# Optimization experiments

Hardware: AMD Instinct MI355X
Metric: run time of the kernel (lower is better)

The kernel has to match this reference:

```python
import jax, jax.numpy as jnp
import numpy as np

B, S, D, C = 2, 4096, 768, 8192
SCALE = 1.0
LN_EPS = 1e-5


def setup_inputs() -> dict:
    key = jax.random.key(0)
    ks = jax.random.split(key, 8)
    std = 0.03
    return {
        "x": jax.random.normal(ks[0], (B, S, D), dtype=jnp.float32),
        "attention_masks": jax.random.randint(ks[1], (B, S), 0, 2).astype(jnp.int32),
        "Wk": jax.random.normal(ks[2], (D, D), dtype=jnp.float32) * std,
        "Wv": jax.random.normal(ks[3], (D, D), dtype=jnp.float32) * std,
        "bv": jnp.zeros((D,), dtype=jnp.float32),
        "Q": jax.random.normal(ks[4], (C, D), dtype=jnp.float32) * std,  # label_representations
        "ln_gamma": jnp.ones((D,), dtype=jnp.float32),
        "ln_beta": jnp.zeros((D,), dtype=jnp.float32),
        "w_out": jax.random.normal(ks[5], (D,), dtype=jnp.float32) * std,  # output_linear.weight [1, D]
        "b_out": jnp.zeros((), dtype=jnp.float32),  # output_linear.bias [1]
    }


def reference(x, attention_masks, Wk, Wv, bv, Q, ln_gamma, ln_beta, w_out, b_out):
    # K, V projections (torch Linear: x @ W.T + b)
    K = jnp.einsum("bsd,ed->bse", x, Wk)
    V = jnp.einsum("bsd,ed->bse", x, Wv) + bv
    # label-query cross-attention scores: [B, C, S]
    scores = jnp.einsum("cd,bsd->bcs", Q, K)
    # additive mask: -inf where attention_masks == 0 (intended semantics of pad/repeat/masked_fill)
    scores = jnp.where(attention_masks[:, None, :] == 0, -jnp.inf, scores)
    attn = jax.nn.softmax(scores / SCALE, axis=2)  # [B, C, S]
    y = jnp.einsum("bcs,bsd->bcd", attn, V)  # [B, C, D]
    # LayerNorm over last dim
    mu = jnp.mean(y, axis=-1, keepdims=True)
    var = jnp.mean((y - mu) ** 2, axis=-1, keepdims=True)
    y = (y - mu) * jax.lax.rsqrt(var + LN_EPS) * ln_gamma + ln_beta
    # elementwise weight-mul-sum output head: [B, C]
    return jnp.einsum("bcd,d->bc", y, w_out) + b_out
```

## Files before the change

### kernel.cpp

```cpp
#include <hip/hip_runtime.h>
#include <hip/hip_bf16.h>
#include <hip/hip_fp16.h>

typedef _Float16 f16x8 __attribute__((ext_vector_type(8)));
typedef _Float16 f16x4 __attribute__((ext_vector_type(4)));
typedef float f32x4 __attribute__((ext_vector_type(4)));

#define AS1 __attribute__((address_space(1)))
#define AS3 __attribute__((address_space(3)))
#define MFMA16(a, b, c) __builtin_amdgcn_mfma_f32_16x16x32_f16(a, b, c, 0, 0, 0)
#define BARRIER asm volatile("s_barrier" ::: "memory")

__global__ __launch_bounds__(256) void maskscan(const int* __restrict__ am,
                                                int* __restrict__ idx,
                                                int* __restrict__ meta) {
  const int b = blockIdx.x, t = threadIdx.x;
  const int* m = am + (size_t)b * 4096;
  int* ix = idx + (size_t)b * 4096;
  __shared__ int cnt[256];
  __shared__ int pre[257];
  int loc[16], c = 0;
#pragma unroll
  for (int j = 0; j < 16; ++j) {
    loc[j] = m[t * 16 + j];
    c += (loc[j] != 0);
  }
  cnt[t] = c;
  __syncthreads();
  if (t == 0) {
    pre[0] = 0;
    for (int i = 0; i < 256; ++i) pre[i + 1] = pre[i] + cnt[i];
  }
  __syncthreads();
  int p = pre[t];
#pragma unroll
  for (int j = 0; j < 16; ++j)
    if (loc[j]) ix[p++] = t * 16 + j;
  const int valid = pre[256];
  int nsp = ((valid + 255) >> 8) << 8;
  if (nsp < 256) nsp = 256;
  for (int j = valid + t; j < nsp; j += 256) ix[j] = -1;
  if (t == 0) { meta[2 * b] = valid; meta[2 * b + 1] = nsp; }
}

__global__ __launch_bounds__(192) void gather_cvt(const float* __restrict__ x,
                                                  const int* __restrict__ idx,
                                                  const int* __restrict__ meta,
                                                  unsigned short* __restrict__ xc) {
  const int b = blockIdx.y, row = blockIdx.x, t = threadIdx.x;
  if (row >= meta[2 * b + 1]) return;
  const int src = idx[(size_t)b * 4096 + row];
  unsigned short* dst = xc + ((size_t)b * 4096 + row) * 768 + t * 4;
  f16x4 h;
  if (src < 0) {
    h[0] = h[1] = h[2] = h[3] = (_Float16)0.0f;
  } else {
    float4 v = *(const float4*)(x + ((size_t)b * 4096 + src) * 768 + t * 4);
    h[0] = (_Float16)v.x; h[1] = (_Float16)v.y; h[2] = (_Float16)v.z; h[3] = (_Float16)v.w;
  }
  *(f16x4*)dst = h;
}

__global__ __launch_bounds__(256) void cvt_f32_f16(const float* __restrict__ in,
                                                   unsigned short* __restrict__ out,
                                                   int n8) {
  int i = blockIdx.x * 256 + threadIdx.x;
  if (i >= n8) return;
  const float4* p = (const float4*)in + 2 * (size_t)i;
  float4 a = p[0], b = p[1];
  f16x8 h;
  h[0] = (_Float16)a.x; h[1] = (_Float16)a.y; h[2] = (_Float16)a.z; h[3] = (_Float16)a.w;
  h[4] = (_Float16)b.x; h[5] = (_Float16)b.y; h[6] = (_Float16)b.z; h[7] = (_Float16)b.w;
  *(f16x8*)(out + (size_t)i * 8) = h;
}

template <int OMODE, bool RBIAS, int EXITD>
__global__ __launch_bounds__(256) void gemm_nt(const unsigned short* __restrict__ A, int lda,
                                               const unsigned short* __restrict__ B, int ldb,
                                               void* __restrict__ Cout, int ldc,
                                               const float* __restrict__ bias,
                                               const int* __restrict__ meta,
                                               int N, int K) {
  const int nbn = N >> 7;
  const int bm = blockIdx.x / nbn, bn = blockIdx.x % nbn;
  if constexpr (EXITD == 1) {
    if (((bm & 31) << 7) >= meta[2 * (bm >> 5) + 1]) return;
  } else if constexpr (EXITD == 2) {
    if (((bn & 31) << 7) >= meta[2 * (bn >> 5) + 1]) return;
  }
  __shared__ __attribute__((aligned(16))) unsigned short As[128 * 64];
  __shared__ __attribute__((aligned(16))) unsigned short Bs[128 * 64];
  const int tid = threadIdx.x;
  const int w = tid >> 6, l = tid & 63;
  const int wr = w >> 1, wc = w & 1;
  const int lr = l & 15, lg = l >> 4;

  const unsigned short* Ab = A + (size_t)bm * 128 * lda;
  const unsigned short* Bb = B + (size_t)bn * 128 * ldb;

  f32x4 acc[4][4] = {};

  auto ldfrag = [&](const unsigned short* base, int row, int kk) {
    int off = row * 128 + kk * 64 + lg * 16;
    off ^= (row & 7) << 4;
    return *(const f16x8*)((const unsigned char*)base + off);
  };

  for (int kt = 0; kt < K; kt += 64) {
#pragma unroll
    for (int i = 0; i < 4; ++i) {
      const int c = i * 256 + w * 64 + l;
      const int row = c >> 3, col = (((c & 7) ^ (row & 7)) << 3);
      __builtin_amdgcn_global_load_lds((const AS1 void*)(Ab + (size_t)row * lda + kt + col),
                                       (AS3 void*)(As + (i * 256 + w * 64) * 8), 16, 0, 0);
    }
#pragma unroll
    for (int i = 0; i < 4; ++i) {
      const int c = i * 256 + w * 64 + l;
      const int row = c >> 3, col = (((c & 7) ^ (row & 7)) << 3);
      __builtin_amdgcn_global_load_lds((const AS1 void*)(Bb + (size_t)row * ldb + kt + col),
                                       (AS3 void*)(Bs + (i * 256 + w * 64) * 8), 16, 0, 0);
    }
    __syncthreads();
#pragma unroll
    for (int kk = 0; kk < 2; ++kk) {
      f16x8 af[4], bf[4];
#pragma unroll
      for (int mi = 0; mi < 4; ++mi) af[mi] = ldfrag(As, wr * 64 + mi * 16 + lr, kk);
#pragma unroll
      for (int ni = 0; ni < 4; ++ni) bf[ni] = ldfrag(Bs, wc * 64 + ni * 16 + lr, kk);
#pragma unroll
      for (int mi = 0; mi < 4; ++mi)
#pragma unroll
        for (int ni = 0; ni < 4; ++ni)
          acc[mi][ni] = __builtin_amdgcn_mfma_f32_16x16x32_f16(af[mi], bf[ni], acc[mi][ni], 0, 0, 0);
    }
    __syncthreads();
  }

#pragma unroll
  for (int mi = 0; mi < 4; ++mi) {
#pragma unroll
    for (int r = 0; r < 4; ++r) {
      const int row = bm * 128 + wr * 64 + mi * 16 + lg * 4 + r;
      const float badd = RBIAS ? bias[row] : 0.0f;
#pragma unroll
      for (int ni = 0; ni < 4; ++ni) {
        const int col = bn * 128 + wc * 64 + ni * 16 + lr;
        float v = acc[mi][ni][r] + badd;
        if constexpr (OMODE == 0)
          ((unsigned short*)Cout)[(size_t)row * ldc + col] =
              __builtin_bit_cast(unsigned short, (_Float16)v);
        else
          ((float*)Cout)[(size_t)row * ldc + col] = v;
      }
    }
  }
}

template <int EPI, int KSP>
__global__ __launch_bounds__(256, 2) void gemmk(
    const unsigned short* __restrict__ A, int lda,
    const unsigned short* __restrict__ B, int ldb,
    unsigned short* __restrict__ Cout, int ldc, size_t sCk,
    const int* __restrict__ meta, int NTfix,
    int XC, int WBM, int WBN) {
  constexpr int RA = 4;
  constexpr int RB = 2;
  constexpr int BUFSZ = 16384 + 8192;
  __shared__ __attribute__((aligned(16))) unsigned char lds[3 * BUFSZ];

  const int tid = threadIdx.x;
  const int wv = tid >> 6, l = tid & 63;
  const int wm = wv >> 1, wn = wv & 1;
  const int lr = l & 15, lg = l >> 4;

  const int ks = blockIdx.y;
  const int valid = meta[0], nsp = meta[1];

  const int bid = blockIdx.x;
  const int xcd = bid & 7, ii = bid >> 3;
  const int bm = (xcd / XC) * WBM + ii / WBN;
  const int bn = (ii % WBN) * XC + (xcd % XC);

  int NT, koff;
  if constexpr (EPI == 2) {
    NT = NTfix; koff = 0;
    if ((bn << 7) >= nsp) return;
  } else {
    NT = (nsp / KSP) >> 5;
    koff = ks * (nsp / KSP);
  }

  const unsigned short* Ab = A + koff + (size_t)bm * 256 * lda;
  const unsigned short* Bb = B + koff + (size_t)(bn * 128) * ldb;

  const int xr = ((lr >> 1) & 3) << 4;
  const int aoff = ((wm * 128 + lr) << 6) + ((lg << 4) ^ xr);
  const int boff = 16384 + ((wn * 64 + lr) << 6) + ((lg << 4) ^ xr);

  const int scol = ((tid & 3) ^ ((tid >> 3) & 3)) << 3;
  const int srow = tid >> 2;
  const unsigned short* sa[RA];
  const unsigned short* sb[RB];
#pragma unroll
  for (int r = 0; r < RA; ++r) sa[r] = Ab + (size_t)(srow + r * 64) * lda + scol;
#pragma unroll
  for (int r = 0; r < RB; ++r) sb[r] = Bb + (size_t)(srow + r * 64) * ldb + scol;
  const int dA = wv * 1024;

  auto stageAll = [&](int eoff, int bo_) {
#pragma unroll
    for (int r = 0; r < RA; ++r)
      __builtin_amdgcn_global_load_lds((const AS1 void*)(sa[r] + eoff),
                                       (AS3 void*)(lds + bo_ + r * 4096 + dA), 16, 0, 0);
#pragma unroll
    for (int r = 0; r < RB; ++r)
      __builtin_amdgcn_global_load_lds((const AS1 void*)(sb[r] + eoff),
                                       (AS3 void*)(lds + bo_ + 16384 + r * 4096 + dA), 16, 0, 0);
  };

  f32x4 acc[8][4] = {};

  stageAll(0, 0);
  stageAll(32, BUFSZ);
  asm volatile("s_waitcnt vmcnt(6)" ::: "memory");
  BARRIER;

  int bo = 0;
  for (int t = 0; t < NT; ++t) {
    const unsigned char* pa = lds + bo + aoff;
    const unsigned char* pb = lds + bo + boff;
    f16x8 a0 = *(const f16x8*)(pa);
    f16x8 a1 = *(const f16x8*)(pa + 1024);
    f16x8 a2 = *(const f16x8*)(pa + 2048);
    f16x8 a3 = *(const f16x8*)(pa + 3072);
    f16x8 b0 = *(const f16x8*)(pb);
    f16x8 b1 = *(const f16x8*)(pb + 1024);
    f16x8 b2 = *(const f16x8*)(pb + 2048);
    f16x8 b3 = *(const f16x8*)(pb + 3072);
    const int bo2 = (bo >= BUFSZ) ? bo - BUFSZ : bo + 2 * BUFSZ;
    if (t + 2 < NT) stageAll((t + 2) * 32, bo2);
    __builtin_amdgcn_s_setprio(1);
    acc[0][0] = MFMA16(a0, b0, acc[0][0]);
    acc[0][1] = MFMA16(a0, b1, acc[0][1]);
    acc[0][2] = MFMA16(a0, b2, acc[0][2]);
    acc[0][3] = MFMA16(a0, b3, acc[0][3]);
    acc[1][0] = MFMA16(a1, b0, acc[1][0]);
    acc[1][1] = MFMA16(a1, b1, acc[1][1]);
    acc[1][2] = MFMA16(a1, b2, acc[1][2]);
    acc[1][3] = MFMA16(a1, b3, acc[1][3]);
    acc[2][0] = MFMA16(a2, b0, acc[2][0]);
    acc[2][1] = MFMA16(a2, b1, acc[2][1]);
    acc[2][2] = MFMA16(a2, b2, acc[2][2]);
    acc[2][3] = MFMA16(a2, b3, acc[2][3]);
    acc[3][0] = MFMA16(a3, b0, acc[3][0]);
    acc[3][1] = MFMA16(a3, b1, acc[3][1]);
    acc[3][2] = MFMA16(a3, b2, acc[3][2]);
    acc[3][3] = MFMA16(a3, b3, acc[3][3]);
    f16x8 a4 = *(const f16x8*)(pa + 4096);
    f16x8 a5 = *(const f16x8*)(pa + 5120);
    f16x8 a6 = *(const f16x8*)(pa + 6144);
    f16x8 a7 = *(const f16x8*)(pa + 7168);
    acc[4][0] = MFMA16(a4, b0, acc[4][0]);
    acc[4][1] = MFMA16(a4, b1, acc[4][1]);
    acc[4][2] = MFMA16(a4, b2, acc[4][2]);
    acc[4][3] = MFMA16(a4, b3, acc[4][3]);
    acc[5][0] = MFMA16(a5, b0, acc[5][0]);
    acc[5][1] = MFMA16(a5, b1, acc[5][1]);
    acc[5][2] = MFMA16(a5, b2, acc[5][2]);
    acc[5][3] = MFMA16(a5, b3, acc[5][3]);
    acc[6][0] = MFMA16(a6, b0, acc[6][0]);
    acc[6][1] = MFMA16(a6, b1, acc[6][1]);
    acc[6][2] = MFMA16(a6, b2, acc[6][2]);
    acc[6][3] = MFMA16(a6, b3, acc[6][3]);
    acc[7][0] = MFMA16(a7, b0, acc[7][0]);
    acc[7][1] = MFMA16(a7, b1, acc[7][1]);
    acc[7][2] = MFMA16(a7, b2, acc[7][2]);
    acc[7][3] = MFMA16(a7, b3, acc[7][3]);
    __builtin_amdgcn_s_setprio(0);
    if (t + 2 < NT) {
      asm volatile("s_waitcnt vmcnt(6)" ::: "memory");
    } else if (t + 1 < NT) {
      asm volatile("s_waitcnt vmcnt(0)" ::: "memory");
    }
    if (t + 1 < NT) BARRIER;
    bo = (bo == 2 * BUFSZ) ? 0 : bo + BUFSZ;
  }

  const size_t crow0 = (size_t)bm * 256 + wm * 128;
  const int ccol0 = bn * 128 + wn * 64;
  unsigned short* Cz = Cout + ks * sCk;
  int mk[4] = {1, 1, 1, 1};
  if constexpr (EPI == 2) {
#pragma unroll
    for (int nf = 0; nf < 4; ++nf)
      mk[nf] = (ccol0 + nf * 16 + lr) < valid;
  }
#pragma unroll
  for (int mf = 0; mf < 8; ++mf) {
#pragma unroll
    for (int rr = 0; rr < 4; ++rr) {
      const size_t rb = (crow0 + mf * 16 + lg * 4 + rr) * (size_t)ldc;
#pragma unroll
      for (int nf = 0; nf < 4; ++nf) {
        const int col = ccol0 + nf * 16 + lr;
        float v = acc[mf][nf][rr];
        if constexpr (EPI == 2) v = mk[nf] ? __expf(v) : 0.0f;
        Cz[rb + col] = __builtin_bit_cast(unsigned short, (_Float16)v);
      }
    }
  }
}

__device__ inline float block_sum(float v, float* sh, int t) {
#pragma unroll
  for (int o = 32; o; o >>= 1) v += __shfl_xor(v, o);
  __syncthreads();
  if ((t & 63) == 0) sh[t >> 6] = v;
  __syncthreads();
  return sh[0] + sh[1] + sh[2] + sh[3];
}

__global__ __launch_bounds__(256) void ln_head(const unsigned short* __restrict__ yp,
                                               size_t koff,
                                               const float* __restrict__ gam,
                                               const float* __restrict__ bet,
                                               const float* __restrict__ wo,
                                               const float* __restrict__ bo,
                                               float* __restrict__ out) {
  const size_t rbase = (size_t)blockIdx.x * 768;
  const _Float16* y0 = (const _Float16*)yp + rbase;
  const _Float16* y1 = y0 + koff;
  const _Float16* y2 = y1 + koff;
  const _Float16* y3 = y2 + koff;
  const int t = threadIdx.x;
  float a0 = (float)y0[t] + (float)y1[t] + (float)y2[t] + (float)y3[t];
  float a1 = (float)y0[t + 256] + (float)y1[t + 256] + (float)y2[t + 256] + (float)y3[t + 256];
  float a2 = (float)y0[t + 512] + (float)y1[t + 512] + (float)y2[t + 512] + (float)y3[t + 512];
  __shared__ float sh[4];
  float s = block_sum(a0 + a1 + a2, sh, t);
  float mu = s * (1.0f / 768.0f);
  float d0 = a0 - mu, d1 = a1 - mu, d2 = a2 - mu;
  float q = block_sum(d0 * d0 + d1 * d1 + d2 * d2, sh, t);
  float rs = rsqrtf(q * (1.0f / 768.0f) + 1e-5f);
  float o = (d0 * rs * gam[t] + bet[t]) * wo[t] +
            (d1 * rs * gam[t + 256] + bet[t + 256]) * wo[t + 256] +
            (d2 * rs * gam[t + 512] + bet[t + 512]) * wo[t + 512];
  o = block_sum(o, sh, t);
  if (t == 0) out[blockIdx.x] = o + bo[0];
}

extern "C" void kernel_launch(void* const* d_in, const int* in_sizes, int n_in,
                              void* d_out, int out_size, void* d_ws, size_t ws_size,
                              hipStream_t stream) {
  const float* x  = (const float*)d_in[0];
  const int*   am = (const int*)d_in[1];
  const float* Wk = (const float*)d_in[2];
  const float* Wv = (const float*)d_in[3];
  const float* bv = (const float*)d_in[4];
  const float* Q  = (const float*)d_in[5];
  const float* gam = (const float*)d_in[6];
  const float* bet = (const float*)d_in[7];
  const float* wo  = (const float*)d_in[8];
  const float* bo  = (const float*)d_in[9];
  float* out = (float*)d_out;

  const int S = 4096, D = 768, C = 8192;
  const size_t nX = (size_t)2 * S * D;
  const size_t nW = (size_t)D * D;
  const size_t nQ = (size_t)C * D;
  const size_t nP = (size_t)C * S;
  const size_t nY = (size_t)C * D;

  unsigned short* xc  = (unsigned short*)d_ws;
  unsigned short* Wkb = xc + nX;
  unsigned short* Wvb = Wkb + nW;
  unsigned short* Qb  = Wvb + nW;
  unsigned short* Kb  = Qb + nQ;
  unsigned short* Vt  = Kb + nX;
  unsigned short* P   = Vt + nX;
  unsigned short* yp  = P + nP;
  int* idx  = (int*)(yp + 4 * nY);
  int* meta = idx + 2 * 4096;

  maskscan<<<2, 256, 0, stream>>>(am, idx, meta);
  gather_cvt<<<dim3(4096, 2), 192, 0, stream>>>(x, idx, meta, xc);

  cvt_f32_f16<<<(int)(nW / 8 / 256), 256, 0, stream>>>(Wk, Wkb, (int)(nW / 8));
  cvt_f32_f16<<<(int)(nW / 8 / 256), 256, 0, stream>>>(Wv, Wvb, (int)(nW / 8));
  cvt_f32_f16<<<(int)(nQ / 8 / 256), 256, 0, stream>>>(Q, Qb, (int)(nQ / 8));

  gemm_nt<0, false, 1><<<(8192 / 128) * (768 / 128), 256, 0, stream>>>(
      xc, D, Wkb, D, Kb, D, nullptr, meta, 768, D);
  gemm_nt<0, true, 2><<<(768 / 128) * (8192 / 128), 256, 0, stream>>>(
      Wvb, D, xc, D, Vt, 2 * S, bv, meta, 2 * S, D);

  for (int b = 0; b < 2; ++b) {
    gemmk<2, 1><<<dim3(1024, 1), 256, 0, stream>>>(
        Qb, D, Kb + (size_t)b * S * D, D, P, S, 0,
        meta + 2 * b, 24, 2, 8, 16);
    gemmk<0, 4><<<dim3(192, 4), 256, 0, stream>>>(
        P, S, Vt + (size_t)b * S, 2 * S, yp, D, nY,
        meta + 2 * b, 0, 2, 8, 3);
    ln_head<<<dim3(C, 1), 256, 0, stream>>>(yp, nY, gam, bet, wo, bo, out + (size_t)b * C);
  }
}
```

Baseline: 247.2 us.

## Replace triple-buffered 256x128 GEMM with simpler single-buffered 128x128 tile kernel

Swaps the attention GEMM kernel from a 256x128 tile with BK=32 triple-buffered async LDS staging to a 128x128 tile with BK=64 and a single LDS buffer synchronised by two barriers per iteration. The grids double to match the smaller tiles, the XCD-aware block mapping is simplified, and the launch-bounds occupancy hint is dropped. This gives more blocks and fewer accumulators per wave, but global-load and MFMA overlap within a block is lost and per-block operand reuse is lower.

```diff
diff --git a/kernel.cpp b/kernel.cpp
--- a/kernel.cpp
+++ b/kernel.cpp
@@ -9,7 +9,6 @@
 #define AS1 __attribute__((address_space(1)))
 #define AS3 __attribute__((address_space(3)))
 #define MFMA16(a, b, c) __builtin_amdgcn_mfma_f32_16x16x32_f16(a, b, c, 0, 0, 0)
-#define BARRIER asm volatile("s_barrier" ::: "memory")
 
 __global__ __launch_bounds__(256) void maskscan(const int* __restrict__ am,
                                                 int* __restrict__ idx,
@@ -159,154 +158,92 @@
 }
 
 template <int EPI, int KSP>
-__global__ __launch_bounds__(256, 2) void gemmk(
+__global__ __launch_bounds__(256) void gemm128(
     const unsigned short* __restrict__ A, int lda,
     const unsigned short* __restrict__ B, int ldb,
     unsigned short* __restrict__ Cout, int ldc, size_t sCk,
-    const int* __restrict__ meta, int NTfix,
-    int XC, int WBM, int WBN) {
-  constexpr int RA = 4;
-  constexpr int RB = 2;
-  constexpr int BUFSZ = 16384 + 8192;
-  __shared__ __attribute__((aligned(16))) unsigned char lds[3 * BUFSZ];
-
+    const int* __restrict__ meta, int NTfix) {
+  __shared__ __attribute__((aligned(16))) unsigned short As[128 * 64];
+  __shared__ __attribute__((aligned(16))) unsigned short Bs[128 * 64];
   const int tid = threadIdx.x;
-  const int wv = tid >> 6, l = tid & 63;
-  const int wm = wv >> 1, wn = wv & 1;
+  const int w = tid >> 6, l = tid & 63;
+  const int wr = w >> 1, wc = w & 1;
   const int lr = l & 15, lg = l >> 4;
 
+  const int valid = meta[0], nsp = meta[1];
   const int ks = blockIdx.y;
-  const int valid = meta[0], nsp = meta[1];
-
   const int bid = blockIdx.x;
   const int xcd = bid & 7, ii = bid >> 3;
-  const int bm = (xcd / XC) * WBM + ii / WBN;
-  const int bn = (ii % WBN) * XC + (xcd % XC);
-
-  int NT, koff;
+
+  int bm, bn, NT, koff;
   if constexpr (EPI == 2) {
-    NT = NTfix; koff = 0;
+    bm = ii >> 2;
+    bn = (ii & 3) * 8 + xcd;
     if ((bn << 7) >= nsp) return;
+    NT = NTfix;
+    koff = 0;
   } else {
-    NT = (nsp / KSP) >> 5;
+    bm = xcd * 8 + ii / 6;
+    bn = ii % 6;
+    NT = (nsp / KSP) >> 6;
     koff = ks * (nsp / KSP);
   }
 
-  const unsigned short* Ab = A + koff + (size_t)bm * 256 * lda;
-  const unsigned short* Bb = B + koff + (size_t)(bn * 128) * ldb;
-
-  const int xr = ((lr >> 1) & 3) << 4;
-  const int aoff = ((wm * 128 + lr) << 6) + ((lg << 4) ^ xr);
-  const int boff = 16384 + ((wn * 64 + lr) << 6) + ((lg << 4) ^ xr);
-
-  const int scol = ((tid & 3) ^ ((tid >> 3) & 3)) << 3;
-  const int srow = tid >> 2;
-  const unsigned short* sa[RA];
-  const unsigned short* sb[RB];
-#pragma unroll
-  for (int r = 0; r < RA; ++r) sa[r] = Ab + (size_t)(srow + r * 64) * lda + scol;
-#pragma unroll
-  for (int r = 0; r < RB; ++r) sb[r] = Bb + (size_t)(srow + r * 64) * ldb + scol;
-  const int dA = wv * 1024;
-
-  auto stageAll = [&](int eoff, int bo_) {
-#pragma unroll
-    for (int r = 0; r < RA; ++r)
-      __builtin_amdgcn_global_load_lds((const AS1 void*)(sa[r] + eoff),
-                                       (AS3 void*)(lds + bo_ + r * 4096 + dA), 16, 0, 0);
-#pragma unroll
-    for (int r = 0; r < RB; ++r)
-      __builtin_amdgcn_global_load_lds((const AS1 void*)(sb[r] + eoff),
-                                       (AS3 void*)(lds + bo_ + 16384 + r * 4096 + dA), 16, 0, 0);
+  const unsigned short* Ab = A + koff + (size_t)bm * 128 * lda;
+  const unsigned short* Bb = B + koff + (size_t)bn * 128 * ldb;
+
+  f32x4 acc[4][4] = {};
+
+  auto ldfrag = [&](const unsigned short* base, int row, int kk) {
+    int off = row * 128 + kk * 64 + lg * 16;
+    off ^= (row & 7) << 4;
+    return *(const f16x8*)((const unsigned char*)base + off);
   };
 
-  f32x4 acc[8][4] = {};
-
-  stageAll(0, 0);
-  stageAll(32, BUFSZ);
-  asm volatile("s_waitcnt vmcnt(6)" ::: "memory");
-  BARRIER;
-
-  int bo = 0;
   for (int t = 0; t < NT; ++t) {
-    const unsigned char* pa = lds + bo + aoff;
-    const unsigned char* pb = lds + bo + boff;
-    f16x8 a0 = *(const f16x8*)(pa);
-    f16x8 a1 = *(const f16x8*)(pa + 1024);
-    f16x8 a2 = *(const f16x8*)(pa + 2048);
-    f16x8 a3 = *(const f16x8*)(pa + 3072);
-    f16x8 b0 = *(const f16x8*)(pb);
-    f16x8 b1 = *(const f16x8*)(pb + 1024);
-    f16x8 b2 = *(const f16x8*)(pb + 2048);
-    f16x8 b3 = *(const f16x8*)(pb + 3072);
-    const int bo2 = (bo >= BUFSZ) ? bo - BUFSZ : bo + 2 * BUFSZ;
-    if (t + 2 < NT) stageAll((t + 2) * 32, bo2);
-    __builtin_amdgcn_s_setprio(1);
-    acc[0][0] = MFMA16(a0, b0, acc[0][0]);
-    acc[0][1] = MFMA16(a0, b1, acc[0][1]);
-    acc[0][2] = MFMA16(a0, b2, acc[0][2]);
-    acc[0][3] = MFMA16(a0, b3, acc[0][3]);
-    acc[1][0] = MFMA16(a1, b0, acc[1][0]);
-    acc[1][1] = MFMA16(a1, b1, acc[1][1]);
-    acc[1][2] = MFMA16(a1, b2, acc[1][2]);
-    acc[1][3] = MFMA16(a1, b3, acc[1][3]);
-    acc[2][0] = MFMA16(a2, b0, acc[2][0]);
-    acc[2][1] = MFMA16(a2, b1, acc[2][1]);
-    acc[2][2] = MFMA16(a2, b2, acc[2][2]);
-    acc[2][3] = MFMA16(a2, b3, acc[2][3]);
-    acc[3][0] = MFMA16(a3, b0, acc[3][0]);
-    acc[3][1] = MFMA16(a3, b1, acc[3][1]);
-    acc[3][2] = MFMA16(a3, b2, acc[3][2]);
-    acc[3][3] = MFMA16(a3, b3, acc[3][3]);
-    f16x8 a4 = *(const f16x8*)(pa + 4096);
-    f16x8 a5 = *(const f16x8*)(pa + 5120);
-    f16x8 a6 = *(const f16x8*)(pa + 6144);
-    f16x8 a7 = *(const f16x8*)(pa + 7168);
-    acc[4][0] = MFMA16(a4, b0, acc[4][0]);
-    acc[4][1] = MFMA16(a4, b1, acc[4][1]);
-    acc[4][2] = MFMA16(a4, b2, acc[4][2]);
-    acc[4][3] = MFMA16(a4, b3, acc[4][3]);
-    acc[5][0] = MFMA16(a5, b0, acc[5][0]);
-    acc[5][1] = MFMA16(a5, b1, acc[5][1]);
-    acc[5][2] = MFMA16(a5, b2, acc[5][2]);
-    acc[5][3] = MFMA16(a5, b3, acc[5][3]);
-    acc[6][0] = MFMA16(a6, b0, acc[6][0]);
-    acc[6][1] = MFMA16(a6, b1, acc[6][1]);
-    acc[6][2] = MFMA16(a6, b2, acc[6][2]);
-    acc[6][3] = MFMA16(a6, b3, acc[6][3]);
-    acc[7][0] = MFMA16(a7, b0, acc[7][0]);
-    acc[7][1] = MFMA16(a7, b1, acc[7][1]);
-    acc[7][2] = MFMA16(a7, b2, acc[7][2]);
-    acc[7][3] = MFMA16(a7, b3, acc[7][3]);
-    __builtin_amdgcn_s_setprio(0);
-    if (t + 2 < NT) {
-      asm volatile("s_waitcnt vmcnt(6)" ::: "memory");
-    } else if (t + 1 < NT) {
-      asm volatile("s_waitcnt vmcnt(0)" ::: "memory");
-    }
-    if (t + 1 < NT) BARRIER;
-    bo = (bo == 2 * BUFSZ) ? 0 : bo + BUFSZ;
-  }
-
-  const size_t crow0 = (size_t)bm * 256 + wm * 128;
-  const int ccol0 = bn * 128 + wn * 64;
-  unsigned short* Cz = Cout + ks * sCk;
-  int mk[4] = {1, 1, 1, 1};
-  if constexpr (EPI == 2) {
-#pragma unroll
-    for (int nf = 0; nf < 4; ++nf)
-      mk[nf] = (ccol0 + nf * 16 + lr) < valid;
-  }
-#pragma unroll
-  for (int mf = 0; mf < 8; ++mf) {
-#pragma unroll
-    for (int rr = 0; rr < 4; ++rr) {
-      const size_t rb = (crow0 + mf * 16 + lg * 4 + rr) * (size_t)ldc;
-#pragma unroll
-      for (int nf = 0; nf < 4; ++nf) {
-        const int col = ccol0 + nf * 16 + lr;
-        float v = acc[mf][nf][rr];
-        if constexpr (EPI == 2) v = mk[nf] ? __expf(v) : 0.0f;
+    const int kt = t * 64;
+#pragma unroll
+    for (int i = 0; i < 4; ++i) {
+      const int c = i * 256 + w * 64 + l;
+      const int row = c >> 3, col = (((c & 7) ^ (row & 7)) << 3);
+      __builtin_amdgcn_global_load_lds((const AS1 void*)(Ab + (size_t)row * lda + kt + col),
+                                       (AS3 void*)(As + (i * 256 + w * 64) * 8), 16, 0, 0);
+    }
+#pragma unroll
+    for (int i = 0; i < 4; ++i) {
+      const int c = i * 256 + w * 64 + l;
+      const int row = c >> 3, col = (((c & 7) ^ (row & 7)) << 3);
+      __builtin_amdgcn_global_load_lds((const AS1 void*)(Bb + (size_t)row * ldb + kt + col),
+                                       (AS3 void*)(Bs + (i * 256 + w * 64) * 8), 16, 0, 0);
+    }
+    __syncthreads();
+#pragma unroll
+    for (int kk = 0; kk < 2; ++kk) {
+      f16x8 af[4], bf[4];
+#pragma unroll
+      for (int mi = 0; mi < 4; ++mi) af[mi] = ldfrag(As, wr * 64 + mi * 16 + lr, kk);
+#pragma unroll
+      for (int ni = 0; ni < 4; ++ni) bf[ni] = ldfrag(Bs, wc * 64 + ni * 16 + lr, kk);
+#pragma unroll
+      for (int mi = 0; mi < 4; ++mi)
+#pragma unroll
+        for (int ni = 0; ni < 4; ++ni)
+          acc[mi][ni] = MFMA16(af[mi], bf[ni], acc[mi][ni]);
+    }
+    __syncthreads();
+  }
+
+  unsigned short* Cz = Cout + (size_t)ks * sCk;
+#pragma unroll
+  for (int mi = 0; mi < 4; ++mi) {
+#pragma unroll
+    for (int r = 0; r < 4; ++r) {
+      const size_t rb = (size_t)(bm * 128 + wr * 64 + mi * 16 + lg * 4 + r) * ldc;
+#pragma unroll
+      for (int ni = 0; ni < 4; ++ni) {
+        const int col = bn * 128 + wc * 64 + ni * 16 + lr;
+        float v = acc[mi][ni][r];
+        if constexpr (EPI == 2) v = (col < valid) ? __expf(v) : 0.0f;
         Cz[rb + col] = __builtin_bit_cast(unsigned short, (_Float16)v);
       }
     }
@@ -397,12 +334,10 @@
       Wvb, D, xc, D, Vt, 2 * S, bv, meta, 2 * S, D);
 
   for (int b = 0; b < 2; ++b) {
-    gemmk<2, 1><<<dim3(1024, 1), 256, 0, stream>>>(
-        Qb, D, Kb + (size_t)b * S * D, D, P, S, 0,
-        meta + 2 * b, 24, 2, 8, 16);
-    gemmk<0, 4><<<dim3(192, 4), 256, 0, stream>>>(
-        P, S, Vt + (size_t)b * S, 2 * S, yp, D, nY,
-        meta + 2 * b, 0, 2, 8, 3);
+    gemm128<2, 1><<<dim3(2048, 1), 256, 0, stream>>>(
+        Qb, D, Kb + (size_t)b * S * D, D, P, S, 0, meta + 2 * b, 12);
+    gemm128<0, 4><<<dim3(384, 4), 256, 0, stream>>>(
+        P, S, Vt + (size_t)b * S, 2 * S, yp, D, nY, meta + 2 * b, 0);
     ln_head<<<dim3(C, 1), 256, 0, stream>>>(yp, nY, gam, bet, wo, bo, out + (size_t)b * C);
   }
 }
```

After: 292.8 us. 1.18x slower.
